# Performance work log

Measured on AMD Instinct MI355X. Metric: run time of the kernel, lower is better.

The kernel has to match this reference:

```python
import jax, jax.numpy as jnp
import numpy as np

I_FEAT = 4096
O_FEAT = 4096
BATCH = 8192


def setup_inputs() -> dict:
    key = jax.random.key(0)
    k1, k2, k3 = jax.random.split(key, 3)
    x_input = jax.random.normal(k1, (BATCH, I_FEAT), dtype=jnp.float32)
    toeplitz_params = jax.random.normal(k2, (O_FEAT + I_FEAT - 1,), dtype=jnp.float32) * (1.0 / np.sqrt(I_FEAT))
    bias = jax.random.normal(k3, (O_FEAT,), dtype=jnp.float32) * (1.0 / np.sqrt(I_FEAT))
    return {"x_input": x_input, "toeplitz_params": toeplitz_params, "bias": bias}


def _toeplitz(params, out_features, in_features):
    # row i, col j -> params[(out_features - 1 - i) + j]
    i = jnp.arange(out_features)[:, None]
    j = jnp.arange(in_features)[None, :]
    return params[(out_features - 1) - i + j]  # [O, I]


def reference(x_input, toeplitz_params, bias):
    weight = _toeplitz(toeplitz_params, O_FEAT, I_FEAT)  # [O, I]
    # x.mm(weight.t()) + bias
    return jnp.einsum('bi,oi->bo', x_input, weight) + bias[None, :]
```

## Files before the change

kernel.cpp:

```cpp
#include <hip/hip_runtime.h>

typedef __attribute__((ext_vector_type(4))) int i32x4;
typedef __attribute__((ext_vector_type(4))) float f32x4;

#define AS1 __attribute__((address_space(1)))
#define AS3 __attribute__((address_space(3)))

constexpr int MDIM = 8192;
constexpr int NDIM = 4096;
constexpr int KDIM = 4096;

constexpr int BM = 256, BN = 256, BKB = 128;
constexpr int NKT = KDIM / BKB;

__device__ __forceinline__ void gld_lds16(const signed char* g, signed char* l) {
  __builtin_amdgcn_global_load_lds((const AS1 void*)g, (AS3 void*)l, 16, 0, 0);
}

__device__ __forceinline__ int q8(float v, float inv) {
  return __float2int_rn(v * inv);
}

__global__ void wscale_kernel(const float* __restrict__ params, float* __restrict__ swbuf) {
  int t = (int)threadIdx.x;
  float m = 0.f;
  for (int i = t; i < NDIM + KDIM - 1; i += 256) m = fmaxf(m, fabsf(params[i]));
#pragma unroll
  for (int off = 32; off >= 1; off >>= 1) m = fmaxf(m, __shfl_xor(m, off));
  __shared__ float red[4];
  if ((t & 63) == 0) red[t >> 6] = m;
  __syncthreads();
  if (t == 0) {
    m = fmaxf(fmaxf(red[0], red[1]), fmaxf(red[2], red[3]));
    m = fmaxf(m, 1e-30f);
    swbuf[0] = m * (1.0f / 127.0f);
    swbuf[1] = 127.0f / m;
  }
}

__global__ __launch_bounds__(256) void quant_x_kernel(
    const float* __restrict__ x, signed char* __restrict__ xq, float* __restrict__ sxr) {
  int row = (int)blockIdx.x;
  int t = (int)threadIdx.x;
  const float4* px = (const float4*)(x + (size_t)row * KDIM) + t * 4;
  float4 v[4];
#pragma unroll
  for (int i = 0; i < 4; ++i) v[i] = px[i];
  float m = 0.f;
#pragma unroll
  for (int i = 0; i < 4; ++i)
    m = fmaxf(fmaxf(fmaxf(fabsf(v[i].x), fabsf(v[i].y)), fmaxf(fabsf(v[i].z), fabsf(v[i].w))), m);
#pragma unroll
  for (int off = 32; off >= 1; off >>= 1) m = fmaxf(m, __shfl_xor(m, off));
  __shared__ float red[4];
  if ((t & 63) == 0) red[t >> 6] = m;
  __syncthreads();
  m = fmaxf(fmaxf(red[0], red[1]), fmaxf(red[2], red[3]));
  m = fmaxf(m, 1e-30f);
  float inv = 127.0f / m;
  if (t == 0) sxr[row] = m * (1.0f / 127.0f);
  i32x4 w;
#pragma unroll
  for (int i = 0; i < 4; ++i) {
    int q0 = q8(v[i].x, inv), q1 = q8(v[i].y, inv), q2 = q8(v[i].z, inv), q3 = q8(v[i].w, inv);
    w[i] = (q0 & 0xff) | ((q1 & 0xff) << 8) | ((q2 & 0xff) << 16) | ((q3 & 0xff) << 24);
  }
  *(i32x4*)(xq + (size_t)row * KDIM + t * 16) = w;
}

__global__ __launch_bounds__(256) void build_wq_kernel(
    const float* __restrict__ params, const float* __restrict__ swbuf,
    signed char* __restrict__ wq) {
  float inv = swbuf[1];
  int i = blockIdx.x * 256 + (int)threadIdx.x;
  int o = i >> 8;
  int k0 = (i & 255) << 4;
  const float* p = params + (NDIM - 1 - o + k0);
  i32x4 w;
#pragma unroll
  for (int j = 0; j < 4; ++j) {
    int q0 = q8(p[4 * j + 0], inv), q1 = q8(p[4 * j + 1], inv);
    int q2 = q8(p[4 * j + 2], inv), q3 = q8(p[4 * j + 3], inv);
    w[j] = (q0 & 0xff) | ((q1 & 0xff) << 8) | ((q2 & 0xff) << 16) | ((q3 & 0xff) << 24);
  }
  *(i32x4*)(wq + (size_t)o * KDIM + k0) = w;
}

__global__ __launch_bounds__(512, 2) void toep_gemm_i8(
    const signed char* __restrict__ A,
    const signed char* __restrict__ Bw,
    const float* __restrict__ bias,
    const float* __restrict__ sxr,
    const float* __restrict__ swbuf,
    float* __restrict__ C)
{
  __shared__ signed char sA[2][BM * BKB];
  __shared__ signed char sB[2][BN * BKB];

  constexpr int NBM = MDIM / BM;
  constexpr int NBN = NDIM / BN;
  constexpr int NWG = NBM * NBN;
  int bid = (int)blockIdx.x;
  int swz = (bid & 7) * (NWG >> 3) + (bid >> 3);
  int bm = swz / NBN, bn = swz % NBN;
  int m0 = bm * BM, n0 = bn * BN;

  int t = (int)threadIdx.x;
  int lane = t & 63, wid = t >> 6;
  int wm = wid >> 2, wn = wid & 3;
  int lr = lane & 15, lk = lane >> 4;

  int scol = (((t & 7) ^ ((t >> 3) & 7)) << 4);
  const signed char* gA = A + (size_t)(m0 + (t >> 3)) * KDIM + scol;
  const signed char* gB = Bw + (size_t)(n0 + (t >> 3)) * KDIM + scol;

#define STG_A(c, kt, R0) gld_lds16(gA + (size_t)(R0) * KDIM + (kt) * BKB, &sA[c][(R0) * BKB + t * 16])
#define STG_B(c, kt, R0) gld_lds16(gB + (size_t)(R0) * KDIM + (kt) * BKB, &sB[c][(R0) * BKB + t * 16])

  int aswz = (lr & 7) << 4;
  int c0 = (lk * 16) ^ aswz;
  int c1 = (64 + lk * 16) ^ aswz;

  i32x4 avA[4][2], avB[4][2];
  i32x4 bvA[2][2], bvB[2][2];
  i32x4 acc[8][4];
#pragma unroll
  for (int i = 0; i < 8; ++i)
#pragma unroll
    for (int j = 0; j < 4; ++j) acc[i][j] = (i32x4){0, 0, 0, 0};

#define LDA_GRP(c, msub, AV) do { \
  _Pragma("unroll") \
  for (int mi = 0; mi < 4; ++mi) { \
    const signed char* p_ = &sA[c][(wm * 128 + (msub) * 64 + mi * 16 + lr) * BKB]; \
    AV[mi][0] = *(const i32x4*)(p_ + c0); \
    AV[mi][1] = *(const i32x4*)(p_ + c1); \
  } } while (0)

#define LDB_GRP(c, nsub, BV) do { \
  _Pragma("unroll") \
  for (int ni = 0; ni < 2; ++ni) { \
    const signed char* p_ = &sB[c][(wn * 64 + (nsub) * 32 + ni * 16 + lr) * BKB]; \
    BV[ni][0] = *(const i32x4*)(p_ + c0); \
    BV[ni][1] = *(const i32x4*)(p_ + c1); \
  } } while (0)

#define MMA_Q(msub, nsub, AV, BV) do { \
  __builtin_amdgcn_s_setprio(1); \
  _Pragma("unroll") \
  for (int mi = 0; mi < 4; ++mi) \
    _Pragma("unroll") \
    for (int ni = 0; ni < 2; ++ni) { \
      acc[(msub) * 4 + mi][(nsub) * 2 + ni] = __builtin_amdgcn_mfma_i32_16x16x64_i8( \
          AV[mi][0], BV[ni][0], acc[(msub) * 4 + mi][(nsub) * 2 + ni], 0, 0, 0); \
      acc[(msub) * 4 + mi][(nsub) * 2 + ni] = __builtin_amdgcn_mfma_i32_16x16x64_i8( \
          AV[mi][1], BV[ni][1], acc[(msub) * 4 + mi][(nsub) * 2 + ni], 0, 0, 0); \
    } \
  __builtin_amdgcn_s_setprio(0); \
} while (0)

#define SB0() __builtin_amdgcn_sched_barrier(0)
#define BAR() __builtin_amdgcn_s_barrier()

  STG_B(0, 0, 0); STG_B(0, 0, 64); STG_B(0, 0, 128); STG_B(0, 0, 192);
  STG_A(0, 0, 0); STG_A(0, 0, 64); STG_A(0, 0, 128); STG_A(0, 0, 192);
  asm volatile("s_waitcnt vmcnt(0)" ::: "memory");
  BAR();
  LDA_GRP(0, 0, avA); LDB_GRP(0, 0, bvA);
  SB0();

#define TILE(c, kt) do { \
  const bool st_ = (kt) + 1 < NKT; \
   \
  LDB_GRP(c, 1, bvB); \
  if (st_) { STG_B((c) ^ 1, (kt) + 1, 0); STG_B((c) ^ 1, (kt) + 1, 64); \
             STG_B((c) ^ 1, (kt) + 1, 128); STG_B((c) ^ 1, (kt) + 1, 192); } \
  SB0(); \
  asm volatile("s_waitcnt lgkmcnt(4)" ::: "memory"); SB0(); \
  MMA_Q(0, 0, avA, bvA); \
   \
  LDA_GRP(c, 1, avB); \
  if (st_) { STG_A((c) ^ 1, (kt) + 1, 0); STG_A((c) ^ 1, (kt) + 1, 64); \
             STG_A((c) ^ 1, (kt) + 1, 128); STG_A((c) ^ 1, (kt) + 1, 192); } \
  SB0(); \
  asm volatile("s_waitcnt lgkmcnt(8)" ::: "memory"); SB0(); \
  MMA_Q(0, 1, avA, bvB); \
   \
  asm volatile("s_waitcnt lgkmcnt(0)" ::: "memory"); SB0(); \
  MMA_Q(1, 0, avB, bvA); \
   \
  if (st_) { asm volatile("s_waitcnt vmcnt(0)" ::: "memory"); } \
  BAR(); \
  if (st_) { LDA_GRP((c) ^ 1, 0, avA); LDB_GRP((c) ^ 1, 0, bvA); SB0(); } \
  MMA_Q(1, 1, avB, bvB); \
} while (0)

  for (int kt = 0; kt < NKT; kt += 2) {
    TILE(0, kt);
    TILE(1, kt + 1);
  }

  float sw = swbuf[0];
  float bvv[4];
#pragma unroll
  for (int fn = 0; fn < 4; ++fn) bvv[fn] = bias[n0 + wn * 64 + fn * 16 + lr];
#pragma unroll
  for (int fm = 0; fm < 8; ++fm) {
    int row0 = m0 + wm * 128 + fm * 16 + lk * 4;
    float sx_[4];
#pragma unroll
    for (int r = 0; r < 4; ++r) sx_[r] = sxr[row0 + r] * sw;
#pragma unroll
    for (int fn = 0; fn < 4; ++fn) {
      int col = n0 + wn * 64 + fn * 16 + lr;
#pragma unroll
      for (int r = 0; r < 4; ++r)
        C[(size_t)(row0 + r) * NDIM + col] = (float)acc[fm][fn][r] * sx_[r] + bvv[fn];
    }
  }
#undef TILE
#undef MMA_Q
#undef LDB_GRP
#undef LDA_GRP
#undef STG_A
#undef STG_B
#undef SB0
#undef BAR
}

__global__ __launch_bounds__(256) void toep_f32_fallback(
    const float* __restrict__ X, const float* __restrict__ P,
    const float* __restrict__ bias, float* __restrict__ C)
{
  constexpr int TM = 64, TN = 64, TK = 32;
  __shared__ float xs[TM][TK + 1];
  __shared__ float win[TN + TK];
  int bm = blockIdx.x / (NDIM / TN);
  int bn = blockIdx.x % (NDIM / TN);
  int m0 = bm * TM, n0 = bn * TN;
  int t = (int)threadIdx.x;
  int tx = t & 15, ty = t >> 4;
  float acc[4][4] = {};
  for (int k0 = 0; k0 < KDIM; k0 += TK) {
    __syncthreads();
    for (int i = t; i < TM * TK; i += 256) {
      int r = i >> 5, c = i & 31;
      xs[r][c] = X[(size_t)(m0 + r) * KDIM + k0 + c];
    }
    if (t < TN + TK - 1) win[t] = P[(NDIM - 1) - n0 - (TN - 1) + k0 + t];
    __syncthreads();
    for (int kk = 0; kk < TK; ++kk) {
      float xv[4];
#pragma unroll
      for (int i = 0; i < 4; ++i) xv[i] = xs[ty * 4 + i][kk];
#pragma unroll
      for (int j = 0; j < 4; ++j) {
        float wv = win[kk + (TN - 1) - (tx * 4 + j)];
#pragma unroll
        for (int i = 0; i < 4; ++i) acc[i][j] += xv[i] * wv;
      }
    }
  }
#pragma unroll
  for (int i = 0; i < 4; ++i)
#pragma unroll
    for (int j = 0; j < 4; ++j)
      C[(size_t)(m0 + ty * 4 + i) * NDIM + n0 + tx * 4 + j] = acc[i][j] + bias[n0 + tx * 4 + j];
}

extern "C" void kernel_launch(void* const* d_in, const int* in_sizes, int n_in,
                              void* d_out, int out_size, void* d_ws, size_t ws_size,
                              hipStream_t stream) {
  const float* x = (const float*)d_in[0];
  const float* params = (const float*)d_in[1];
  const float* bias = (const float*)d_in[2];
  float* out = (float*)d_out;

  const size_t xq_off = 0;
  const size_t wq_off = (size_t)MDIM * KDIM;
  const size_t sx_off = wq_off + (size_t)NDIM * KDIM;
  const size_t sw_off = sx_off + (size_t)MDIM * 4;
  const size_t need = sw_off + 64;

  if (ws_size >= need) {
    signed char* xq = (signed char*)d_ws + xq_off;
    signed char* wq = (signed char*)d_ws + wq_off;
    float* sxr = (float*)((char*)d_ws + sx_off);
    float* swbuf = (float*)((char*)d_ws + sw_off);
    wscale_kernel<<<1, 256, 0, stream>>>(params, swbuf);
    quant_x_kernel<<<MDIM, 256, 0, stream>>>(x, xq, sxr);
    build_wq_kernel<<<NDIM * KDIM / 16 / 256, 256, 0, stream>>>(params, swbuf, wq);
    toep_gemm_i8<<<(MDIM / BM) * (NDIM / BN), 512, 0, stream>>>(xq, wq, bias, sxr, swbuf, out);
  } else {
    toep_f32_fallback<<<(MDIM / 64) * (NDIM / 64), 256, 0, stream>>>(x, params, bias, out);
  }
}
```

Measured before the change: 173.6 us.

## Read Toeplitz weights directly from replicated quantized params instead of materializing W

Result: slower. 200.7 us (+15.6%).

```diff
diff --git a/kernel.cpp b/kernel.cpp
--- a/kernel.cpp
+++ b/kernel.cpp
@@ -1,7 +1,6 @@
 #include <hip/hip_runtime.h>
 
 typedef __attribute__((ext_vector_type(4))) int i32x4;
-typedef __attribute__((ext_vector_type(4))) float f32x4;
 
 #define AS1 __attribute__((address_space(1)))
 #define AS3 __attribute__((address_space(3)))
@@ -12,6 +11,7 @@
 
 constexpr int BM = 256, BN = 256, BKB = 128;
 constexpr int NKT = KDIM / BKB;
+constexpr int REP_DW = 2112;
 
 __device__ __forceinline__ void gld_lds16(const signed char* g, signed char* l) {
   __builtin_amdgcn_global_load_lds((const AS1 void*)g, (AS3 void*)l, 16, 0, 0);
@@ -21,21 +21,34 @@
   return __float2int_rn(v * inv);
 }
 
-__global__ void wscale_kernel(const float* __restrict__ params, float* __restrict__ swbuf) {
+__global__ __launch_bounds__(256) void prep_kernel(
+    const float* __restrict__ params, float* __restrict__ swbuf,
+    int* __restrict__ pq_rep) {
+  __shared__ signed char pql[8192 + 8];
+  __shared__ float red[4];
   int t = (int)threadIdx.x;
   float m = 0.f;
   for (int i = t; i < NDIM + KDIM - 1; i += 256) m = fmaxf(m, fabsf(params[i]));
 #pragma unroll
   for (int off = 32; off >= 1; off >>= 1) m = fmaxf(m, __shfl_xor(m, off));
-  __shared__ float red[4];
   if ((t & 63) == 0) red[t >> 6] = m;
   __syncthreads();
-  if (t == 0) {
-    m = fmaxf(fmaxf(red[0], red[1]), fmaxf(red[2], red[3]));
-    m = fmaxf(m, 1e-30f);
-    swbuf[0] = m * (1.0f / 127.0f);
-    swbuf[1] = 127.0f / m;
-  }
+  m = fmaxf(fmaxf(red[0], red[1]), fmaxf(red[2], red[3]));
+  m = fmaxf(m, 1e-30f);
+  float inv = 127.0f / m;
+  if (t == 0) swbuf[0] = m * (1.0f / 127.0f);
+  for (int i = t; i < 8192 + 8; i += 256)
+    pql[i] = (i < NDIM + KDIM - 1) ? (signed char)q8(params[i], inv) : (signed char)0;
+  __syncthreads();
+#pragma unroll
+  for (int r = 0; r < 4; ++r)
+    for (int j = t; j < REP_DW; j += 256) {
+      int b0 = (unsigned char)pql[4 * j + r + 0];
+      int b1 = (unsigned char)pql[4 * j + r + 1];
+      int b2 = (unsigned char)pql[4 * j + r + 2];
+      int b3 = (unsigned char)pql[4 * j + r + 3];
+      pq_rep[r * REP_DW + j] = b0 | (b1 << 8) | (b2 << 16) | (b3 << 24);
+    }
 }
 
 __global__ __launch_bounds__(256) void quant_x_kernel(
@@ -68,34 +81,15 @@
   *(i32x4*)(xq + (size_t)row * KDIM + t * 16) = w;
 }
 
-__global__ __launch_bounds__(256) void build_wq_kernel(
-    const float* __restrict__ params, const float* __restrict__ swbuf,
-    signed char* __restrict__ wq) {
-  float inv = swbuf[1];
-  int i = blockIdx.x * 256 + (int)threadIdx.x;
-  int o = i >> 8;
-  int k0 = (i & 255) << 4;
-  const float* p = params + (NDIM - 1 - o + k0);
-  i32x4 w;
-#pragma unroll
-  for (int j = 0; j < 4; ++j) {
-    int q0 = q8(p[4 * j + 0], inv), q1 = q8(p[4 * j + 1], inv);
-    int q2 = q8(p[4 * j + 2], inv), q3 = q8(p[4 * j + 3], inv);
-    w[j] = (q0 & 0xff) | ((q1 & 0xff) << 8) | ((q2 & 0xff) << 16) | ((q3 & 0xff) << 24);
-  }
-  *(i32x4*)(wq + (size_t)o * KDIM + k0) = w;
-}
-
 __global__ __launch_bounds__(512, 2) void toep_gemm_i8(
     const signed char* __restrict__ A,
-    const signed char* __restrict__ Bw,
+    const int* __restrict__ pq_rep,
     const float* __restrict__ bias,
     const float* __restrict__ sxr,
     const float* __restrict__ swbuf,
     float* __restrict__ C)
 {
   __shared__ signed char sA[2][BM * BKB];
-  __shared__ signed char sB[2][BN * BKB];
 
   constexpr int NBM = MDIM / BM;
   constexpr int NBN = NDIM / BN;
@@ -112,14 +106,15 @@
 
   int scol = (((t & 7) ^ ((t >> 3) & 7)) << 4);
   const signed char* gA = A + (size_t)(m0 + (t >> 3)) * KDIM + scol;
-  const signed char* gB = Bw + (size_t)(n0 + (t >> 3)) * KDIM + scol;
 
 #define STG_A(c, kt, R0) gld_lds16(gA + (size_t)(R0) * KDIM + (kt) * BKB, &sA[c][(R0) * BKB + t * 16])
-#define STG_B(c, kt, R0) gld_lds16(gB + (size_t)(R0) * KDIM + (kt) * BKB, &sB[c][(R0) * BKB + t * 16])
 
   int aswz = (lr & 7) << 4;
   int c0 = (lk * 16) ^ aswz;
   int c1 = (64 + lk * 16) ^ aswz;
+
+  int idx0 = 4095 - (n0 + wn * 64 + lr) + lk * 16;
+  const int* pqb = pq_rep + (idx0 & 3) * REP_DW + (idx0 >> 2);
 
   i32x4 avA[4][2], avB[4][2];
   i32x4 bvA[2][2], bvB[2][2];
@@ -137,13 +132,16 @@
     AV[mi][1] = *(const i32x4*)(p_ + c1); \
   } } while (0)
 
-#define LDB_GRP(c, nsub, BV) do { \
+#define LDB_GRP(BV, NSUB, TDW) do { \
   _Pragma("unroll") \
-  for (int ni = 0; ni < 2; ++ni) { \
-    const signed char* p_ = &sB[c][(wn * 64 + (nsub) * 32 + ni * 16 + lr) * BKB]; \
-    BV[ni][0] = *(const i32x4*)(p_ + c0); \
-    BV[ni][1] = *(const i32x4*)(p_ + c1); \
-  } } while (0)
+  for (int ni = 0; ni < 2; ++ni) \
+    _Pragma("unroll") \
+    for (int h = 0; h < 2; ++h) { \
+      const int* q_ = pqb + ((TDW) - 8 * (NSUB) - 4 * ni + 16 * h); \
+      BV[ni][h][0] = q_[0]; BV[ni][h][1] = q_[1]; \
+      BV[ni][h][2] = q_[2]; BV[ni][h][3] = q_[3]; \
+    } \
+} while (0)
 
 #define MMA_Q(msub, nsub, AV, BV) do { \
   __builtin_amdgcn_s_setprio(1); \
@@ -162,36 +160,37 @@
 #define SB0() __builtin_amdgcn_sched_barrier(0)
 #define BAR() __builtin_amdgcn_s_barrier()
 
-  STG_B(0, 0, 0); STG_B(0, 0, 64); STG_B(0, 0, 128); STG_B(0, 0, 192);
+  LDB_GRP(bvA, 0, 0); SB0();
   STG_A(0, 0, 0); STG_A(0, 0, 64); STG_A(0, 0, 128); STG_A(0, 0, 192);
   asm volatile("s_waitcnt vmcnt(0)" ::: "memory");
   BAR();
-  LDA_GRP(0, 0, avA); LDB_GRP(0, 0, bvA);
-  SB0();
+  LDA_GRP(0, 0, avA); SB0();
 
 #define TILE(c, kt) do { \
   const bool st_ = (kt) + 1 < NKT; \
-   \
-  LDB_GRP(c, 1, bvB); \
-  if (st_) { STG_B((c) ^ 1, (kt) + 1, 0); STG_B((c) ^ 1, (kt) + 1, 64); \
-             STG_B((c) ^ 1, (kt) + 1, 128); STG_B((c) ^ 1, (kt) + 1, 192); } \
-  SB0(); \
-  asm volatile("s_waitcnt lgkmcnt(4)" ::: "memory"); SB0(); \
+  LDB_GRP(bvB, 1, 0); SB0(); \
+  if (st_) { STG_A((c) ^ 1, (kt) + 1, 0); STG_A((c) ^ 1, (kt) + 1, 64); \
+             STG_A((c) ^ 1, (kt) + 1, 128); STG_A((c) ^ 1, (kt) + 1, 192); SB0(); } \
+  LDA_GRP(c, 1, avB); SB0(); \
+   \
+  if (st_) { asm volatile("s_waitcnt vmcnt(20)" ::: "memory"); } \
+  else     { asm volatile("s_waitcnt vmcnt(16)" ::: "memory"); } \
+  asm volatile("s_waitcnt lgkmcnt(8)" ::: "memory"); SB0(); \
   MMA_Q(0, 0, avA, bvA); \
-   \
-  LDA_GRP(c, 1, avB); \
-  if (st_) { STG_A((c) ^ 1, (kt) + 1, 0); STG_A((c) ^ 1, (kt) + 1, 64); \
-             STG_A((c) ^ 1, (kt) + 1, 128); STG_A((c) ^ 1, (kt) + 1, 192); } \
-  SB0(); \
-  asm volatile("s_waitcnt lgkmcnt(8)" ::: "memory"); SB0(); \
-  MMA_Q(0, 1, avA, bvB); \
    \
   asm volatile("s_waitcnt lgkmcnt(0)" ::: "memory"); SB0(); \
   MMA_Q(1, 0, avB, bvA); \
    \
-  if (st_) { asm volatile("s_waitcnt vmcnt(0)" ::: "memory"); } \
+  if (st_) { LDB_GRP(bvA, 0, 32); SB0(); } \
+   \
+  if (st_) { asm volatile("s_waitcnt vmcnt(20)" ::: "memory"); } \
+  else     { asm volatile("s_waitcnt vmcnt(0)" ::: "memory"); } \
+  SB0(); \
+  MMA_Q(0, 1, avA, bvB); \
+   \
+  if (st_) { asm volatile("s_waitcnt vmcnt(16)" ::: "memory"); } \
   BAR(); \
-  if (st_) { LDA_GRP((c) ^ 1, 0, avA); LDB_GRP((c) ^ 1, 0, bvA); SB0(); } \
+  if (st_) { LDA_GRP((c) ^ 1, 0, avA); SB0(); pqb += 32; } \
   MMA_Q(1, 1, avB, bvB); \
 } while (0)
 
@@ -223,7 +222,6 @@
 #undef LDB_GRP
 #undef LDA_GRP
 #undef STG_A
-#undef STG_B
 #undef SB0
 #undef BAR
 }
@@ -277,20 +275,19 @@
   float* out = (float*)d_out;
 
   const size_t xq_off = 0;
-  const size_t wq_off = (size_t)MDIM * KDIM;
-  const size_t sx_off = wq_off + (size_t)NDIM * KDIM;
+  const size_t pq_off = (size_t)MDIM * KDIM;
+  const size_t sx_off = pq_off + 4 * REP_DW * 4 + 64;
   const size_t sw_off = sx_off + (size_t)MDIM * 4;
   const size_t need = sw_off + 64;
 
   if (ws_size >= need) {
     signed char* xq = (signed char*)d_ws + xq_off;
-    signed char* wq = (signed char*)d_ws + wq_off;
+    int* pq_rep = (int*)((char*)d_ws + pq_off);
     float* sxr = (float*)((char*)d_ws + sx_off);
     float* swbuf = (float*)((char*)d_ws + sw_off);
-    wscale_kernel<<<1, 256, 0, stream>>>(params, swbuf);
+    prep_kernel<<<1, 256, 0, stream>>>(params, swbuf, pq_rep);
     quant_x_kernel<<<MDIM, 256, 0, stream>>>(x, xq, sxr);
-    build_wq_kernel<<<NDIM * KDIM / 16 / 256, 256, 0, stream>>>(params, swbuf, wq);
-    toep_gemm_i8<<<(MDIM / BM) * (NDIM / BN), 512, 0, stream>>>(xq, wq, bias, sxr, swbuf, out);
+    toep_gemm_i8<<<(MDIM / BM) * (NDIM / BN), 512, 0, stream>>>(xq, pq_rep, bias, sxr, swbuf, out);
   } else {
     toep_f32_fallback<<<(MDIM / 64) * (NDIM / 64), 256, 0, stream>>>(x, params, bias, out);
   }
```
